# Kernel tuning notes

Hardware: AMD Instinct MI355X
Metric: run time of the kernel (lower is better)

Reference implementation:

```python
import jax, jax.numpy as jnp
import numpy as np

N, E, H, L = 50000, 800000, 64, 4
IN_NODE, IN_EDGE = 16, 8


def _lin(x, W, b=None):
    y = x @ W
    return y if b is None else y + b


def setup_inputs() -> dict:
    key = jax.random.key(0)
    ks = jax.random.split(key, 32)
    r = lambda i, shp, s=0.1: jax.random.normal(ks[i], shp, dtype=jnp.float32) * s
    inp = {
        "h": r(0, (N, IN_NODE), 1.0),
        "x": r(1, (N, 3), 1.0),
        "edge_attr": r(2, (E, IN_EDGE), 1.0),
        "node_mask": jnp.ones((N, 1), jnp.float32),
        "edge_mask": jnp.ones((E, 1), jnp.float32),
        # embedding linears
        "Wn_in": r(3, (IN_NODE, H)), "bn_in": r(4, (H,)),
        "Wn_out": r(5, (H, IN_NODE)), "bn_out": r(6, (IN_NODE,)),
        "We_in": r(7, (IN_EDGE, H)), "be_in": r(8, (H,)),
        "We_out": r(9, (H, IN_EDGE)), "be_out": r(10, (IN_EDGE,)),
        # per-layer E_GCL params (stacked over L layers)
        "eW1": r(11, (L, 2 * H + 1 + H, H)), "eb1": r(12, (L, H)),
        "eW2": r(13, (L, H, H)), "eb2": r(14, (L, H)),
        "nW1": r(15, (L, 2 * H, H)), "nb1": r(16, (L, H)),
        "nW2": r(17, (L, H, H)), "nb2": r(18, (L, H)),
        "cW1": r(19, (L, H, H)), "cb1": r(20, (L, H)),
        "cW2": r(21, (L, H, 1)),
        "edge_index": jax.random.randint(ks[22], (2, E), 0, N, dtype=jnp.int32),
    }
    return inp


def reference(h, x, edge_attr, node_mask, edge_mask,
              Wn_in, bn_in, Wn_out, bn_out, We_in, be_in, We_out, be_out,
              eW1, eb1, eW2, eb2, nW1, nb1, nW2, nb2, cW1, cb1, cW2,
              edge_index):
    silu = jax.nn.silu
    n = h.shape[0]
    row, col = edge_index[0], edge_index[1]
    h = _lin(h, Wn_in, bn_in)            # node embedding [N,H]
    e = _lin(edge_attr, We_in, be_in)    # edge embedding [E,H]
    for i in range(eW1.shape[0]):        # n_layers (structural loop)
        coord_diff = x[row] - x[col]                          # [E,3]
        radial = jnp.sum(coord_diff * coord_diff, -1, keepdims=True)  # [E,1]
        coord_diff = coord_diff / (jnp.sqrt(radial) + 1.0)    # norm_diff
        # edge model: gather -> MLP
        m = jnp.concatenate([h[row], h[col], radial, e], axis=-1)
        m = silu(_lin(m, eW1[i], eb1[i]))
        m = silu(_lin(m, eW2[i], eb2[i]))
        m = m * edge_mask
        # coord model (tanh=False, agg='sum'): scatter-add translations
        trans = coord_diff * _lin(silu(_lin(m, cW1[i], cb1[i])), cW2[i])
        x = x + jax.ops.segment_sum(trans, row, num_segments=n)
        # node model: scatter-add messages, MLP, residual (recurrent)
        agg = jax.ops.segment_sum(m, row, num_segments=n)
        out = _lin(silu(_lin(jnp.concatenate([h, agg], -1), nW1[i], nb1[i])), nW2[i], nb2[i])
        h = (h + out) * node_mask
        x = x * node_mask
        e = m  # edge_update: carry message as updated edge feature
    e = _lin(e, We_out, be_out) * edge_mask
    h = _lin(h, Wn_out, bn_out) * node_mask
    return h, x, e
```

## Files before the change

### kernel.cpp

```cpp
#include <hip/hip_runtime.h>

#define N_NODES 50000
#define N_EDGES 800000
#define NLAYERS 4
#define NTILES (N_EDGES / 64)
#define NTILES2 (N_EDGES / 128)

#define K1PAD 224
#define TPITCH 72
#define SCHUNK 49

typedef short bf16x8 __attribute__((ext_vector_type(8)));
typedef float f32x4 __attribute__((ext_vector_type(4)));

__device__ __forceinline__ unsigned short f2b(float f) {
  union { float f; unsigned int u; } v; v.f = f;
  unsigned int u = v.u;
  return (unsigned short)((u + 0x7fffu + ((u >> 16) & 1u)) >> 16);
}
__device__ __forceinline__ float b2f(unsigned short s) {
  union { unsigned int u; float f; } v; v.u = ((unsigned int)s) << 16;
  return v.f;
}
__device__ __forceinline__ float silu_f(float x) {
  return x / (1.0f + __expf(-x));
}

__global__ void k_hist(const int* __restrict__ eidx, int* __restrict__ cnt) {
  int e = blockIdx.x * 256 + threadIdx.x;
  if (e >= N_EDGES) return;
  atomicAdd(&cnt[eidx[e]], 1);
}
__global__ __launch_bounds__(1024) void k_scan(const int* __restrict__ cnt,
                                               int* __restrict__ rowptr,
                                               int* __restrict__ cur) {
  __shared__ int part[1024];
  const int t = threadIdx.x;
  const int base = t * SCHUNK;
  int s = 0;
  for (int i = 0; i < SCHUNK; i++) {
    int idx = base + i;
    s += (idx < N_NODES) ? cnt[idx] : 0;
  }
  part[t] = s;
  __syncthreads();
  for (int off = 1; off < 1024; off <<= 1) {
    int v = (t >= off) ? part[t - off] : 0;
    __syncthreads();
    part[t] += v;
    __syncthreads();
  }
  int run = (t == 0) ? 0 : part[t - 1];
  for (int i = 0; i < SCHUNK; i++) {
    int idx = base + i;
    if (idx < N_NODES) {
      rowptr[idx] = run;
      cur[idx] = run;
      run += cnt[idx];
    }
  }
  if (t == 1023) rowptr[N_NODES] = part[1023];
}
__global__ void k_scatter(const int* __restrict__ eidx, const float* __restrict__ emask,
                          int* __restrict__ cur, int* __restrict__ elist,
                          int* __restrict__ rs, int* __restrict__ cs,
                          float* __restrict__ msrt) {
  int e = blockIdx.x * 256 + threadIdx.x;
  if (e >= N_EDGES) return;
  int r = eidx[e], c = eidx[N_EDGES + e];
  int slot = atomicAdd(&cur[r], 1);
  elist[slot] = e;
  rs[slot] = r;
  cs[slot] = c;
  msrt[slot] = emask[e];
}

__global__ void k_convW1(const float* __restrict__ eW1, unsigned short* __restrict__ Wt1) {
  int id = blockIdx.x * 256 + threadIdx.x;
  if (id >= NLAYERS * 64 * K1PAD) return;
  int k = id % K1PAD; int rem = id / K1PAD; int o = rem % 64; int l = rem / 64;
  int src = (k < 128) ? k : (k < 192 ? k + 1 : (k == 192 ? 128 : -1));
  float v = (src >= 0) ? eW1[((size_t)l * 193 + src) * 64 + o] : 0.0f;
  Wt1[id] = f2b(v);
}
__global__ void k_convT(const float* __restrict__ W, unsigned short* __restrict__ Wt, int K) {
  int id = blockIdx.x * 256 + threadIdx.x;
  if (id >= NLAYERS * 64 * K) return;
  int k = id % K; int rem = id / K; int o = rem % 64; int l = rem / 64;
  Wt[id] = f2b(W[((size_t)l * K + k) * 64 + o]);
}
__global__ void k_convHead(const float* __restrict__ W, unsigned short* __restrict__ Wt, int O) {
  int id = blockIdx.x * 256 + threadIdx.x;
  if (id >= 16 * 64) return;
  int k = id & 63, o = id >> 6;
  Wt[id] = (o < O) ? f2b(W[(size_t)k * O + o]) : (unsigned short)0;
}

__global__ void k_h0(const float* __restrict__ hin, const float* __restrict__ W,
                     const float* __restrict__ b, float* __restrict__ h,
                     unsigned short* __restrict__ hbf) {
  int id = blockIdx.x * 256 + threadIdx.x;
  if (id >= N_NODES * 64) return;
  int n = id >> 6, j = id & 63;
  float s = b[j];
#pragma unroll
  for (int k = 0; k < 16; k++) s += hin[n * 16 + k] * W[k * 64 + j];
  h[id] = s;
  hbf[id] = f2b(s);
}
__global__ void k_e0(const float* __restrict__ ea, const float* __restrict__ W,
                     const float* __restrict__ b, const int* __restrict__ elist,
                     unsigned short* __restrict__ ebuf) {
  int id = blockIdx.x * 256 + threadIdx.x;
  if (id >= N_EDGES * 64) return;
  int pos = id >> 6, j = id & 63;
  int e = elist[pos];
  float s = b[j];
#pragma unroll
  for (int k = 0; k < 8; k++) s += ea[e * 8 + k] * W[k * 64 + j];
  ebuf[id] = f2b(s);
}

__global__ __launch_bounds__(256) void edge_kernel(
    const unsigned short* __restrict__ hbf, unsigned short* __restrict__ ebuf,
    const float* __restrict__ xin, float* __restrict__ xout,
    float* __restrict__ agg,
    const int* __restrict__ rs, const int* __restrict__ cs,
    const float* __restrict__ msrt,
    const unsigned short* __restrict__ Wt1,
    const unsigned short* __restrict__ Wt2,
    const unsigned short* __restrict__ Wtc,
    const float* __restrict__ eb1, const float* __restrict__ eb2,
    const float* __restrict__ cb1, const float* __restrict__ cw2) {
  __shared__ __attribute__((aligned(16))) unsigned short sT[128 * TPITCH];
  __shared__ __attribute__((aligned(16))) unsigned short sM[128 * TPITCH];
  __shared__ float sNdx[128 * 3];
  __shared__ float sMaskS[128];
  __shared__ int sRow[128];

  const int qq = NTILES2 >> 3, r8 = NTILES2 & 7;
  const int xcd = blockIdx.x & 7, sidx = blockIdx.x >> 3;
  const int tile = (xcd < r8 ? xcd * (qq + 1) : r8 * (qq + 1) + (xcd - r8) * qq) + sidx;

  const int t = threadIdx.x;
  const int lane = t & 63, w = t >> 6;
  const int q = lane >> 4, li = lane & 15;
  const int rowA = w * 32 + li;
  const int rowB = rowA + 16;
  const int e0 = tile * 128 + rowA;
  const int e1 = e0 + 16;

  const int rA = rs[e0], cA = cs[e0];
  const int rB = rs[e1], cB = cs[e1];

  float radA = 0.f, radB = 0.f;
  if (q == 0) {
    {
      float dx0 = xin[rA * 3 + 0] - xin[cA * 3 + 0];
      float dx1 = xin[rA * 3 + 1] - xin[cA * 3 + 1];
      float dx2 = xin[rA * 3 + 2] - xin[cA * 3 + 2];
      radA = dx0 * dx0 + dx1 * dx1 + dx2 * dx2;
      float inv = 1.0f / (sqrtf(radA) + 1.0f);
      sRow[rowA] = rA;
      sMaskS[rowA] = msrt[e0];
      sNdx[rowA * 3 + 0] = dx0 * inv;
      sNdx[rowA * 3 + 1] = dx1 * inv;
      sNdx[rowA * 3 + 2] = dx2 * inv;
    }
    {
      float dx0 = xin[rB * 3 + 0] - xin[cB * 3 + 0];
      float dx1 = xin[rB * 3 + 1] - xin[cB * 3 + 1];
      float dx2 = xin[rB * 3 + 2] - xin[cB * 3 + 2];
      radB = dx0 * dx0 + dx1 * dx1 + dx2 * dx2;
      float inv = 1.0f / (sqrtf(radB) + 1.0f);
      sRow[rowB] = rB;
      sMaskS[rowB] = msrt[e1];
      sNdx[rowB * 3 + 0] = dx0 * inv;
      sNdx[rowB * 3 + 1] = dx1 * inv;
      sNdx[rowB * 3 + 2] = dx2 * inv;
    }
  }

  const unsigned short* hrA = hbf + (size_t)rA * 64;
  const unsigned short* hcA = hbf + (size_t)cA * 64;
  const unsigned short* epA = ebuf + (size_t)e0 * 64;
  const unsigned short* hrB = hbf + (size_t)rB * 64;
  const unsigned short* hcB = hbf + (size_t)cB * 64;
  const unsigned short* epB = ebuf + (size_t)e1 * 64;

  f32x4 accA[4], accB[4];
  const f32x4 zero4 = {0.f, 0.f, 0.f, 0.f};
#pragma unroll
  for (int ct = 0; ct < 4; ct++) { accA[ct] = zero4; accB[ct] = zero4; }

  {
    bf16x8 afA[7], afB[7];
    afA[0] = *(const bf16x8*)(hrA + q * 8);
    afA[1] = *(const bf16x8*)(hrA + 32 + q * 8);
    afA[2] = *(const bf16x8*)(hcA + q * 8);
    afA[3] = *(const bf16x8*)(hcA + 32 + q * 8);
    afA[4] = *(const bf16x8*)(epA + q * 8);
    afA[5] = *(const bf16x8*)(epA + 32 + q * 8);
    afB[0] = *(const bf16x8*)(hrB + q * 8);
    afB[1] = *(const bf16x8*)(hrB + 32 + q * 8);
    afB[2] = *(const bf16x8*)(hcB + q * 8);
    afB[3] = *(const bf16x8*)(hcB + 32 + q * 8);
    afB[4] = *(const bf16x8*)(epB + q * 8);
    afB[5] = *(const bf16x8*)(epB + 32 + q * 8);
    bf16x8 a6A = {0, 0, 0, 0, 0, 0, 0, 0};
    bf16x8 a6B = {0, 0, 0, 0, 0, 0, 0, 0};
    if (q == 0) { a6A[0] = (short)f2b(radA); a6B[0] = (short)f2b(radB); }
    afA[6] = a6A; afB[6] = a6B;
#pragma unroll
    for (int ks = 0; ks < 7; ks++) {
      int kb = ks * 32 + q * 8;
#pragma unroll
      for (int ct = 0; ct < 4; ct++) {
        bf16x8 bfr = *(const bf16x8*)(Wt1 + (size_t)(ct * 16 + li) * K1PAD + kb);
        accA[ct] = __builtin_amdgcn_mfma_f32_16x16x32_bf16(afA[ks], bfr, accA[ct], 0, 0, 0);
        accB[ct] = __builtin_amdgcn_mfma_f32_16x16x32_bf16(afB[ks], bfr, accB[ct], 0, 0, 0);
      }
    }
  }
#pragma unroll
  for (int ct = 0; ct < 4; ct++) {
    float bias = eb1[ct * 16 + li];
#pragma unroll
    for (int r2 = 0; r2 < 4; r2++) {
      int elA = w * 32 + q * 4 + r2;
      sT[elA * TPITCH + ct * 16 + li] = f2b(silu_f(accA[ct][r2] + bias));
      sT[(elA + 16) * TPITCH + ct * 16 + li] = f2b(silu_f(accB[ct][r2] + bias));
    }
  }

#pragma unroll
  for (int ct = 0; ct < 4; ct++) { accA[ct] = zero4; accB[ct] = zero4; }
#pragma unroll
  for (int ks = 0; ks < 2; ks++) {
    int kb = ks * 32 + q * 8;
    bf16x8 afA = *(const bf16x8*)(sT + rowA * TPITCH + kb);
    bf16x8 afB = *(const bf16x8*)(sT + rowB * TPITCH + kb);
#pragma unroll
    for (int ct = 0; ct < 4; ct++) {
      bf16x8 bfr = *(const bf16x8*)(Wt2 + (size_t)(ct * 16 + li) * 64 + kb);
      accA[ct] = __builtin_amdgcn_mfma_f32_16x16x32_bf16(afA, bfr, accA[ct], 0, 0, 0);
      accB[ct] = __builtin_amdgcn_mfma_f32_16x16x32_bf16(afB, bfr, accB[ct], 0, 0, 0);
    }
  }
#pragma unroll
  for (int ct = 0; ct < 4; ct++) {
    float bias = eb2[ct * 16 + li];
#pragma unroll
    for (int r2 = 0; r2 < 4; r2++) {
      int elA = w * 32 + q * 4 + r2;
      int elB = elA + 16;
      float vA = silu_f(accA[ct][r2] + bias) * sMaskS[elA];
      float vB = silu_f(accB[ct][r2] + bias) * sMaskS[elB];
      sM[elA * TPITCH + ct * 16 + li] = f2b(vA);
      sM[elB * TPITCH + ct * 16 + li] = f2b(vB);
    }
  }

  {
    int el2 = t >> 1, part = t & 1;
    const uint4* src = (const uint4*)(sM + el2 * TPITCH + part * 32);
    uint4* dst = (uint4*)(ebuf + (size_t)(tile * 128 + el2) * 64 + part * 32);
    dst[0] = src[0]; dst[1] = src[1]; dst[2] = src[2]; dst[3] = src[3];
  }

  {
    float accv = 0.f;
    int curRow = sRow[w * 32];
#pragma unroll
    for (int i = 0; i < 32; i++) {
      int rr = sRow[w * 32 + i];
      float v = b2f(sM[(w * 32 + i) * TPITCH + lane]);
      if (rr != curRow) {
        atomicAdd(&agg[(size_t)curRow * 64 + lane], accv);
        accv = 0.f;
        curRow = rr;
      }
      accv += v;
    }
    atomicAdd(&agg[(size_t)curRow * 64 + lane], accv);
  }

#pragma unroll
  for (int ct = 0; ct < 4; ct++) { accA[ct] = zero4; accB[ct] = zero4; }
#pragma unroll
  for (int ks = 0; ks < 2; ks++) {
    int kb = ks * 32 + q * 8;
    bf16x8 afA = *(const bf16x8*)(sM + rowA * TPITCH + kb);
    bf16x8 afB = *(const bf16x8*)(sM + rowB * TPITCH + kb);
#pragma unroll
    for (int ct = 0; ct < 4; ct++) {
      bf16x8 bfr = *(const bf16x8*)(Wtc + (size_t)(ct * 16 + li) * 64 + kb);
      accA[ct] = __builtin_amdgcn_mfma_f32_16x16x32_bf16(afA, bfr, accA[ct], 0, 0, 0);
      accB[ct] = __builtin_amdgcn_mfma_f32_16x16x32_bf16(afB, bfr, accB[ct], 0, 0, 0);
    }
  }
  float pA[4] = {0.f, 0.f, 0.f, 0.f};
  float pB[4] = {0.f, 0.f, 0.f, 0.f};
#pragma unroll
  for (int ct = 0; ct < 4; ct++) {
    float bias = cb1[ct * 16 + li];
    float wv = cw2[ct * 16 + li];
#pragma unroll
    for (int r2 = 0; r2 < 4; r2++) {
      pA[r2] += silu_f(accA[ct][r2] + bias) * wv;
      pB[r2] += silu_f(accB[ct][r2] + bias) * wv;
    }
  }
#pragma unroll
  for (int m = 1; m < 16; m <<= 1) {
#pragma unroll
    for (int r2 = 0; r2 < 4; r2++) {
      pA[r2] += __shfl_xor(pA[r2], m, 64);
      pB[r2] += __shfl_xor(pB[r2], m, 64);
    }
  }
  if (li < 3) {
    {
      int el0 = w * 32 + q * 4;
      float accx = sNdx[el0 * 3 + li] * pA[0];
      int cr = sRow[el0];
#pragma unroll
      for (int r2 = 1; r2 < 4; r2++) {
        int el = el0 + r2;
        int rr = sRow[el];
        float tv = sNdx[el * 3 + li] * pA[r2];
        if (rr != cr) {
          atomicAdd(&xout[(size_t)cr * 3 + li], accx);
          accx = 0.f;
          cr = rr;
        }
        accx += tv;
      }
      atomicAdd(&xout[(size_t)cr * 3 + li], accx);
    }
    {
      int el0 = w * 32 + 16 + q * 4;
      float accx = sNdx[el0 * 3 + li] * pB[0];
      int cr = sRow[el0];
#pragma unroll
      for (int r2 = 1; r2 < 4; r2++) {
        int el = el0 + r2;
        int rr = sRow[el];
        float tv = sNdx[el * 3 + li] * pB[r2];
        if (rr != cr) {
          atomicAdd(&xout[(size_t)cr * 3 + li], accx);
          accx = 0.f;
          cr = rr;
        }
        accx += tv;
      }
      atomicAdd(&xout[(size_t)cr * 3 + li], accx);
    }
  }
}

__global__ __launch_bounds__(256) void node_kernel(
    float* __restrict__ h, unsigned short* __restrict__ hbf,
    const float* __restrict__ agg,
    float* __restrict__ xout, const float* __restrict__ nmask,
    const unsigned short* __restrict__ Wtn1,
    const unsigned short* __restrict__ Wtn2,
    const float* __restrict__ nb1, const float* __restrict__ nb2) {
  __shared__ __attribute__((aligned(16))) unsigned short sT[64 * TPITCH];
  const int t = threadIdx.x;
  const int nb = blockIdx.x * 64;

  if (t < 192) {
    int n2 = nb + t / 3, c2 = t % 3;
    if (n2 < N_NODES) xout[(size_t)n2 * 3 + c2] *= nmask[n2];
  }

  const int lane = t & 63, w = t >> 6;
  const int q = lane >> 4, li = lane & 15;
  const int nrow = w * 16 + li;
  const int n = nb + nrow;
  const bool valid = (n < N_NODES);
  const f32x4 zero4 = {0.f, 0.f, 0.f, 0.f};

  f32x4 acc[4];
#pragma unroll
  for (int ct = 0; ct < 4; ct++) acc[ct] = zero4;

  {
    bf16x8 afs[4];
    const bf16x8 az = {0, 0, 0, 0, 0, 0, 0, 0};
    if (valid) {
      afs[0] = *(const bf16x8*)(hbf + (size_t)n * 64 + q * 8);
      afs[1] = *(const bf16x8*)(hbf + (size_t)n * 64 + 32 + q * 8);
      const float* ap = agg + (size_t)n * 64;
      bf16x8 a2, a3;
#pragma unroll
      for (int j = 0; j < 8; j++) {
        a2[j] = (short)f2b(ap[q * 8 + j]);
        a3[j] = (short)f2b(ap[32 + q * 8 + j]);
      }
      afs[2] = a2; afs[3] = a3;
    } else {
      afs[0] = az; afs[1] = az; afs[2] = az; afs[3] = az;
    }
#pragma unroll
    for (int ks = 0; ks < 4; ks++) {
      int kb = ks * 32 + q * 8;
#pragma unroll
      for (int ct = 0; ct < 4; ct++) {
        bf16x8 bfr = *(const bf16x8*)(Wtn1 + (size_t)(ct * 16 + li) * 128 + kb);
        acc[ct] = __builtin_amdgcn_mfma_f32_16x16x32_bf16(afs[ks], bfr, acc[ct], 0, 0, 0);
      }
    }
  }
#pragma unroll
  for (int ct = 0; ct < 4; ct++) {
    float bias = nb1[ct * 16 + li];
#pragma unroll
    for (int r2 = 0; r2 < 4; r2++) {
      int nl = w * 16 + q * 4 + r2;
      sT[nl * TPITCH + ct * 16 + li] = f2b(silu_f(acc[ct][r2] + bias));
    }
  }

#pragma unroll
  for (int ct = 0; ct < 4; ct++) acc[ct] = zero4;
#pragma unroll
  for (int ks = 0; ks < 2; ks++) {
    int kb = ks * 32 + q * 8;
    bf16x8 af = *(const bf16x8*)(sT + nrow * TPITCH + kb);
#pragma unroll
    for (int ct = 0; ct < 4; ct++) {
      bf16x8 bfr = *(const bf16x8*)(Wtn2 + (size_t)(ct * 16 + li) * 64 + kb);
      acc[ct] = __builtin_amdgcn_mfma_f32_16x16x32_bf16(af, bfr, acc[ct], 0, 0, 0);
    }
  }
#pragma unroll
  for (int ct = 0; ct < 4; ct++) {
    float bias = nb2[ct * 16 + li];
#pragma unroll
    for (int r2 = 0; r2 < 4; r2++) {
      int node = nb + w * 16 + q * 4 + r2;
      if (node < N_NODES) {
        float nm = nmask[node];
        size_t o = (size_t)node * 64 + ct * 16 + li;
        float hv = (h[o] + acc[ct][r2] + bias) * nm;
        h[o] = hv;
        hbf[o] = f2b(hv);
      }
    }
  }
}

__global__ __launch_bounds__(256) void k_hout(const unsigned short* __restrict__ hbf,
                                              const unsigned short* __restrict__ WoT,
                                              const float* __restrict__ b,
                                              const float* __restrict__ nmask,
                                              float* __restrict__ out) {
  const int t = threadIdx.x, lane = t & 63, w = t >> 6;
  const int q = lane >> 4, li = lane & 15;
  const int nb = blockIdx.x * 64;
  const int n = nb + w * 16 + li;
  const bf16x8 az = {0, 0, 0, 0, 0, 0, 0, 0};
  bf16x8 a0 = az, a1 = az;
  if (n < N_NODES) {
    a0 = *(const bf16x8*)(hbf + (size_t)n * 64 + q * 8);
    a1 = *(const bf16x8*)(hbf + (size_t)n * 64 + 32 + q * 8);
  }
  bf16x8 b0 = *(const bf16x8*)(WoT + li * 64 + q * 8);
  bf16x8 b1 = *(const bf16x8*)(WoT + li * 64 + 32 + q * 8);
  f32x4 acc = {0.f, 0.f, 0.f, 0.f};
  acc = __builtin_amdgcn_mfma_f32_16x16x32_bf16(a0, b0, acc, 0, 0, 0);
  acc = __builtin_amdgcn_mfma_f32_16x16x32_bf16(a1, b1, acc, 0, 0, 0);
  float bias = b[li];
#pragma unroll
  for (int r2 = 0; r2 < 4; r2++) {
    int node = nb + w * 16 + q * 4 + r2;
    if (node < N_NODES) out[(size_t)node * 16 + li] = (acc[r2] + bias) * nmask[node];
  }
}
__global__ __launch_bounds__(256) void k_eout(const unsigned short* __restrict__ ebuf,
                                              const unsigned short* __restrict__ WoT,
                                              const float* __restrict__ b,
                                              const float* __restrict__ emask,
                                              const int* __restrict__ elist,
                                              float* __restrict__ out) {
  const int t = threadIdx.x, lane = t & 63, w = t >> 6;
  const int q = lane >> 4, li = lane & 15;
  const int eb0 = blockIdx.x * 64;
  const int e = eb0 + w * 16 + li;
  bf16x8 a0 = *(const bf16x8*)(ebuf + (size_t)e * 64 + q * 8);
  bf16x8 a1 = *(const bf16x8*)(ebuf + (size_t)e * 64 + 32 + q * 8);
  bf16x8 b0 = *(const bf16x8*)(WoT + li * 64 + q * 8);
  bf16x8 b1 = *(const bf16x8*)(WoT + li * 64 + 32 + q * 8);
  f32x4 acc = {0.f, 0.f, 0.f, 0.f};
  acc = __builtin_amdgcn_mfma_f32_16x16x32_bf16(a0, b0, acc, 0, 0, 0);
  acc = __builtin_amdgcn_mfma_f32_16x16x32_bf16(a1, b1, acc, 0, 0, 0);
  if (li < 8) {
    float bias = b[li];
#pragma unroll
    for (int r2 = 0; r2 < 4; r2++) {
      int ee = eb0 + w * 16 + q * 4 + r2;
      int orig = elist[ee];
      out[(size_t)orig * 8 + li] = (acc[r2] + bias) * emask[orig];
    }
  }
}

extern "C" void kernel_launch(void* const* d_in, const int* in_sizes, int n_in,
                              void* d_out, int out_size, void* d_ws, size_t ws_size,
                              hipStream_t stream) {
  (void)in_sizes; (void)n_in; (void)out_size; (void)ws_size;
  const float* in_h   = (const float*)d_in[0];
  const float* in_x   = (const float*)d_in[1];
  const float* in_ea  = (const float*)d_in[2];
  const float* nmask  = (const float*)d_in[3];
  const float* emask  = (const float*)d_in[4];
  const float* Wn_in  = (const float*)d_in[5];
  const float* bn_in  = (const float*)d_in[6];
  const float* Wn_out = (const float*)d_in[7];
  const float* bn_out = (const float*)d_in[8];
  const float* We_in  = (const float*)d_in[9];
  const float* be_in  = (const float*)d_in[10];
  const float* We_out = (const float*)d_in[11];
  const float* be_out = (const float*)d_in[12];
  const float* eW1    = (const float*)d_in[13];
  const float* eb1    = (const float*)d_in[14];
  const float* eW2    = (const float*)d_in[15];
  const float* eb2    = (const float*)d_in[16];
  const float* nW1    = (const float*)d_in[17];
  const float* nb1    = (const float*)d_in[18];
  const float* nW2    = (const float*)d_in[19];
  const float* nb2    = (const float*)d_in[20];
  const float* cW1    = (const float*)d_in[21];
  const float* cb1    = (const float*)d_in[22];
  const float* cW2    = (const float*)d_in[23];
  const int*   eidx   = (const int*)d_in[24];

  char* ws = (char*)d_ws;
  size_t off = 0;
  auto alloc = [&](size_t bytes) {
    size_t o = off; off = (off + bytes + 255) & ~(size_t)255; return (void*)(ws + o);
  };
  float* h             = (float*)alloc((size_t)N_NODES * 64 * 4);
  unsigned short* hbf  = (unsigned short*)alloc((size_t)N_NODES * 64 * 2);
  unsigned short* ebuf = (unsigned short*)alloc((size_t)N_EDGES * 64 * 2);
  float* agg           = (float*)alloc((size_t)N_NODES * 64 * 4);
  float* xb0           = (float*)alloc((size_t)N_NODES * 3 * 4);
  float* xb1           = (float*)alloc((size_t)N_NODES * 3 * 4);
  int* cnt             = (int*)alloc((size_t)N_NODES * 4);
  int* rowptr          = (int*)alloc((size_t)(N_NODES + 1) * 4);
  int* cur             = (int*)alloc((size_t)N_NODES * 4);
  int* elist           = (int*)alloc((size_t)N_EDGES * 4);
  int* rsorted         = (int*)alloc((size_t)N_EDGES * 4);
  int* csorted         = (int*)alloc((size_t)N_EDGES * 4);
  float* msorted       = (float*)alloc((size_t)N_EDGES * 4);
  unsigned short* Wt1  = (unsigned short*)alloc((size_t)NLAYERS * 64 * K1PAD * 2);
  unsigned short* Wt2  = (unsigned short*)alloc((size_t)NLAYERS * 64 * 64 * 2);
  unsigned short* Wtc  = (unsigned short*)alloc((size_t)NLAYERS * 64 * 64 * 2);
  unsigned short* Wtn1 = (unsigned short*)alloc((size_t)NLAYERS * 64 * 128 * 2);
  unsigned short* Wtn2 = (unsigned short*)alloc((size_t)NLAYERS * 64 * 64 * 2);
  unsigned short* WoN  = (unsigned short*)alloc((size_t)16 * 64 * 2);
  unsigned short* WoE  = (unsigned short*)alloc((size_t)16 * 64 * 2);

  hipMemsetAsync(cnt, 0, (size_t)N_NODES * 4, stream);
  k_hist<<<(N_EDGES + 255) / 256, 256, 0, stream>>>(eidx, cnt);
  k_scan<<<1, 1024, 0, stream>>>(cnt, rowptr, cur);
  k_scatter<<<(N_EDGES + 255) / 256, 256, 0, stream>>>(eidx, emask, cur, elist,
                                                       rsorted, csorted, msorted);

  k_convW1<<<(NLAYERS * 64 * K1PAD + 255) / 256, 256, 0, stream>>>(eW1, Wt1);
  k_convT<<<(NLAYERS * 64 * 64 + 255) / 256, 256, 0, stream>>>(eW2, Wt2, 64);
  k_convT<<<(NLAYERS * 64 * 64 + 255) / 256, 256, 0, stream>>>(cW1, Wtc, 64);
  k_convT<<<(NLAYERS * 64 * 128 + 255) / 256, 256, 0, stream>>>(nW1, Wtn1, 128);
  k_convT<<<(NLAYERS * 64 * 64 + 255) / 256, 256, 0, stream>>>(nW2, Wtn2, 64);
  k_convHead<<<4, 256, 0, stream>>>(Wn_out, WoN, 16);
  k_convHead<<<4, 256, 0, stream>>>(We_out, WoE, 8);

  k_h0<<<(N_NODES * 64 + 255) / 256, 256, 0, stream>>>(in_h, Wn_in, bn_in, h, hbf);
  k_e0<<<(N_EDGES * 64 + 255) / 256, 256, 0, stream>>>(in_ea, We_in, be_in, elist, ebuf);
  hipMemcpyAsync(xb0, in_x, (size_t)N_NODES * 3 * 4, hipMemcpyDeviceToDevice, stream);

  for (int l = 0; l < NLAYERS; l++) {
    float* xi = (l & 1) ? xb1 : xb0;
    float* xo = (l & 1) ? xb0 : xb1;
    hipMemsetAsync(agg, 0, (size_t)N_NODES * 64 * 4, stream);
    hipMemcpyAsync(xo, xi, (size_t)N_NODES * 3 * 4, hipMemcpyDeviceToDevice, stream);
    edge_kernel<<<NTILES2, 256, 0, stream>>>(
        hbf, ebuf, xi, xo, agg, rsorted, csorted, msorted,
        Wt1 + (size_t)l * 64 * K1PAD, Wt2 + (size_t)l * 64 * 64, Wtc + (size_t)l * 64 * 64,
        eb1 + l * 64, eb2 + l * 64, cb1 + l * 64, cW2 + l * 64);
    node_kernel<<<(N_NODES + 63) / 64, 256, 0, stream>>>(
        h, hbf, agg, xo, nmask,
        Wtn1 + (size_t)l * 64 * 128, Wtn2 + (size_t)l * 64 * 64, nb1 + l * 64, nb2 + l * 64);
  }

  float* out = (float*)d_out;
  k_hout<<<(N_NODES + 63) / 64, 256, 0, stream>>>(hbf, WoN, bn_out, nmask, out);
  k_eout<<<NTILES, 256, 0, stream>>>(ebuf, WoE, be_out, emask, elist, out + 950000);
  hipMemcpyAsync(out + 800000, xb0, (size_t)N_NODES * 3 * 4, hipMemcpyDeviceToDevice, stream);
}
```

Baseline: 1.336 ms.

## Fuse agg zeroing and x-buffer copies into node kernel, add MFMA setprio

The node kernel now zeroes each node's agg row right after reading it, and writes the masked coordinates into both the current and the next-layer x buffer. This removes the per-layer memset of agg and the device-to-device copy of x, and the final x copy to the output. The edge kernel also raises wave priority around its MFMA loops with s_setprio, so matrix work is favoured when waves compete. This relies on the node kernel covering every node so agg ends up fully zeroed for the next layer.

Measured after the change: 1.354 ms. Within noise of the previous version (+1.4%).

```diff
diff --git a/kernel.cpp b/kernel.cpp
--- a/kernel.cpp
+++ b/kernel.cpp
@@ -211,6 +211,7 @@
     bf16x8 a6B = {0, 0, 0, 0, 0, 0, 0, 0};
     if (q == 0) { a6A[0] = (short)f2b(radA); a6B[0] = (short)f2b(radB); }
     afA[6] = a6A; afB[6] = a6B;
+    __builtin_amdgcn_s_setprio(1);
 #pragma unroll
     for (int ks = 0; ks < 7; ks++) {
       int kb = ks * 32 + q * 8;
@@ -221,6 +222,7 @@
         accB[ct] = __builtin_amdgcn_mfma_f32_16x16x32_bf16(afB[ks], bfr, accB[ct], 0, 0, 0);
       }
     }
+    __builtin_amdgcn_s_setprio(0);
   }
 #pragma unroll
   for (int ct = 0; ct < 4; ct++) {
@@ -235,6 +237,7 @@
 
 #pragma unroll
   for (int ct = 0; ct < 4; ct++) { accA[ct] = zero4; accB[ct] = zero4; }
+  __builtin_amdgcn_s_setprio(1);
 #pragma unroll
   for (int ks = 0; ks < 2; ks++) {
     int kb = ks * 32 + q * 8;
@@ -247,6 +250,7 @@
       accB[ct] = __builtin_amdgcn_mfma_f32_16x16x32_bf16(afB, bfr, accB[ct], 0, 0, 0);
     }
   }
+  __builtin_amdgcn_s_setprio(0);
 #pragma unroll
   for (int ct = 0; ct < 4; ct++) {
     float bias = eb2[ct * 16 + li];
@@ -287,6 +291,7 @@
 
 #pragma unroll
   for (int ct = 0; ct < 4; ct++) { accA[ct] = zero4; accB[ct] = zero4; }
+  __builtin_amdgcn_s_setprio(1);
 #pragma unroll
   for (int ks = 0; ks < 2; ks++) {
     int kb = ks * 32 + q * 8;
@@ -299,6 +304,7 @@
       accB[ct] = __builtin_amdgcn_mfma_f32_16x16x32_bf16(afB, bfr, accB[ct], 0, 0, 0);
     }
   }
+  __builtin_amdgcn_s_setprio(0);
   float pA[4] = {0.f, 0.f, 0.f, 0.f};
   float pB[4] = {0.f, 0.f, 0.f, 0.f};
 #pragma unroll
@@ -361,8 +367,9 @@
 
 __global__ __launch_bounds__(256) void node_kernel(
     float* __restrict__ h, unsigned short* __restrict__ hbf,
-    const float* __restrict__ agg,
-    float* __restrict__ xout, const float* __restrict__ nmask,
+    float* __restrict__ agg,
+    float* __restrict__ xout, float* __restrict__ xnext,
+    const float* __restrict__ nmask,
     const unsigned short* __restrict__ Wtn1,
     const unsigned short* __restrict__ Wtn2,
     const float* __restrict__ nb1, const float* __restrict__ nb2) {
@@ -372,7 +379,12 @@
 
   if (t < 192) {
     int n2 = nb + t / 3, c2 = t % 3;
-    if (n2 < N_NODES) xout[(size_t)n2 * 3 + c2] *= nmask[n2];
+    if (n2 < N_NODES) {
+      size_t o = (size_t)n2 * 3 + c2;
+      float v = xout[o] * nmask[n2];
+      xout[o] = v;
+      xnext[o] = v;
+    }
   }
 
   const int lane = t & 63, w = t >> 6;
@@ -381,6 +393,7 @@
   const int n = nb + nrow;
   const bool valid = (n < N_NODES);
   const f32x4 zero4 = {0.f, 0.f, 0.f, 0.f};
+  const float4 f4z = make_float4(0.f, 0.f, 0.f, 0.f);
 
   f32x4 acc[4];
 #pragma unroll
@@ -392,7 +405,7 @@
     if (valid) {
       afs[0] = *(const bf16x8*)(hbf + (size_t)n * 64 + q * 8);
       afs[1] = *(const bf16x8*)(hbf + (size_t)n * 64 + 32 + q * 8);
-      const float* ap = agg + (size_t)n * 64;
+      float* ap = agg + (size_t)n * 64;
       bf16x8 a2, a3;
 #pragma unroll
       for (int j = 0; j < 8; j++) {
@@ -400,6 +413,10 @@
         a3[j] = (short)f2b(ap[32 + q * 8 + j]);
       }
       afs[2] = a2; afs[3] = a3;
+      *(float4*)(ap + q * 8) = f4z;
+      *(float4*)(ap + q * 8 + 4) = f4z;
+      *(float4*)(ap + 32 + q * 8) = f4z;
+      *(float4*)(ap + 32 + q * 8 + 4) = f4z;
     } else {
       afs[0] = az; afs[1] = az; afs[2] = az; afs[3] = az;
     }
@@ -563,6 +580,8 @@
   unsigned short* WoN  = (unsigned short*)alloc((size_t)16 * 64 * 2);
   unsigned short* WoE  = (unsigned short*)alloc((size_t)16 * 64 * 2);
 
+  float* out = (float*)d_out;
+
   hipMemsetAsync(cnt, 0, (size_t)N_NODES * 4, stream);
   k_hist<<<(N_EDGES + 255) / 256, 256, 0, stream>>>(eidx, cnt);
   k_scan<<<1, 1024, 0, stream>>>(cnt, rowptr, cur);
@@ -580,23 +599,22 @@
   k_h0<<<(N_NODES * 64 + 255) / 256, 256, 0, stream>>>(in_h, Wn_in, bn_in, h, hbf);
   k_e0<<<(N_EDGES * 64 + 255) / 256, 256, 0, stream>>>(in_ea, We_in, be_in, elist, ebuf);
   hipMemcpyAsync(xb0, in_x, (size_t)N_NODES * 3 * 4, hipMemcpyDeviceToDevice, stream);
+  hipMemcpyAsync(xb1, in_x, (size_t)N_NODES * 3 * 4, hipMemcpyDeviceToDevice, stream);
+  hipMemsetAsync(agg, 0, (size_t)N_NODES * 64 * 4, stream);
 
   for (int l = 0; l < NLAYERS; l++) {
     float* xi = (l & 1) ? xb1 : xb0;
     float* xo = (l & 1) ? xb0 : xb1;
-    hipMemsetAsync(agg, 0, (size_t)N_NODES * 64 * 4, stream);
-    hipMemcpyAsync(xo, xi, (size_t)N_NODES * 3 * 4, hipMemcpyDeviceToDevice, stream);
     edge_kernel<<<NTILES2, 256, 0, stream>>>(
         hbf, ebuf, xi, xo, agg, rsorted, csorted, msorted,
         Wt1 + (size_t)l * 64 * K1PAD, Wt2 + (size_t)l * 64 * 64, Wtc + (size_t)l * 64 * 64,
         eb1 + l * 64, eb2 + l * 64, cb1 + l * 64, cW2 + l * 64);
+    float* xnext = (l == NLAYERS - 1) ? (out + 800000) : xi;
     node_kernel<<<(N_NODES + 63) / 64, 256, 0, stream>>>(
-        h, hbf, agg, xo, nmask,
+        h, hbf, agg, xo, xnext, nmask,
         Wtn1 + (size_t)l * 64 * 128, Wtn2 + (size_t)l * 64 * 64, nb1 + l * 64, nb2 + l * 64);
   }
 
-  float* out = (float*)d_out;
   k_hout<<<(N_NODES + 63) / 64, 256, 0, stream>>>(hbf, WoN, bn_out, nmask, out);
   k_eout<<<NTILES, 256, 0, stream>>>(ebuf, WoE, be_out, emask, elist, out + 950000);
-  hipMemcpyAsync(out + 800000, xb0, (size_t)N_NODES * 3 * 4, hipMemcpyDeviceToDevice, stream);
-}
+}
```
